# Kernel tuning notes

Measured on AMD Instinct MI355X. Metric: run time of the kernel, lower is better.

The kernel has to match this reference:

```python
import jax, jax.numpy as jnp
import numpy as np

NUM_TAGS = 5

def setup_inputs() -> dict:
    key = jax.random.key(0)
    ks = jax.random.split(key, 8)
    B, N, K, Q = 2, 5, 5, 4
    Ls, Lq, D = 128, 128, 768
    inp = {
        'support_token_embedding': jax.random.normal(ks[0], (B * N * K, Ls, D), jnp.float32),
        'query_token_embedding': jax.random.normal(ks[1], (B * N * Q, Lq, D), jnp.float32),
        'support_mask': jnp.ones((B * N * K, Ls), jnp.float32),
        'query_mask': jnp.ones((B * N * Q, Lq), jnp.float32),
        'support_entity_label': jax.random.normal(ks[2], (B * N * K, Ls, NUM_TAGS), jnp.float32),
        'proj_w': jax.random.normal(ks[3], (D, 4 * D), jnp.float32) * 0.02,
        'proj_b': jnp.zeros((D,), jnp.float32),
        'rel_w1': jax.random.normal(ks[4], (D, 4 * D), jnp.float32) * 0.02,
        'rel_b1': jnp.zeros((D,), jnp.float32),
        'rel_w2': jax.random.normal(ks[5], (1, D), jnp.float32) * 0.02,
        'rel_b2': jnp.zeros((1,), jnp.float32),
        'B': B, 'N': N, 'K': K, 'Q': Q,
    }
    return inp

def _fuse(m1, m2):
    return jnp.concatenate([m1, m2, jnp.abs(m1 - m2), m1 * m2], axis=-1)

def reference(support_token_embedding, query_token_embedding, support_mask, query_mask,
              support_entity_label, proj_w, proj_b, rel_w1, rel_b1, rel_w2, rel_b2,
              B, N, K, Q):
    D = support_token_embedding.shape[-1]
    Lq = query_token_embedding.shape[1]

    # ---- cal_bio: per-(sample,shot) tag prototypes, vectorized ----
    labels = jnp.argmax(support_entity_label, axis=-1)                 # [BNK, Ls]
    onehot = jax.nn.one_hot(labels, NUM_TAGS, dtype=jnp.float32)       # [BNK, Ls, T]
    # tag 0 ('O') is additionally gated by the support mask
    masks = jnp.concatenate([onehot[:, :, :1] * support_mask[:, :, None], onehot[:, :, 1:]], axis=2)
    sums = jnp.einsum('blt,bld->btd', masks, support_token_embedding)  # [BNK, T, D]
    cnt = jnp.sum(masks, axis=1)[:, :, None]                           # [BNK, T, 1]
    proto = jnp.where(cnt > 0, sums / jnp.maximum(cnt, 1.0), 0.0)      # [BNK, T, D]
    proto = proto.reshape(B * N, K, NUM_TAGS, D).mean(axis=1)          # mean over K shots
    proto = proto.reshape(B, N, NUM_TAGS, D)                           # support_BIO

    # ---- expand to all (query, class) pairs: batch = B*N*Q*N ----
    BQ = B * N * Q * N
    support = jnp.broadcast_to(proto[:, None], (B, N * Q, N, NUM_TAGS, D)).reshape(BQ, NUM_TAGS, D)
    query = jnp.broadcast_to(query_token_embedding.reshape(B, N * Q, 1, Lq, D),
                             (B, N * Q, N, Lq, D)).reshape(BQ, Lq, D)
    qmask = jnp.broadcast_to(query_mask.reshape(B, N * Q, 1, Lq),
                             (B, N * Q, N, Lq)).reshape(BQ, Lq, 1)
    smask = jnp.ones((BQ, NUM_TAGS, 1), jnp.float32)

    # ---- CoAttention with additive mask bias + post-softmax mask multiply ----
    att = jnp.einsum('bsd,bqd->bsq', support, query) + smask * jnp.swapaxes(qmask, 1, 2) * 100.0
    support_ = jnp.einsum('bsq,bqd->bsd', jax.nn.softmax(att, axis=2), query) * smask
    query_ = jnp.einsum('bqs,bsd->bqd', jax.nn.softmax(jnp.swapaxes(att, 1, 2), axis=2), support) * qmask

    # ---- fuse + proj + relu ----
    es = jax.nn.relu(_fuse(support, support_) @ proj_w.T + proj_b)     # [BQ, T, D]
    eq = jax.nn.relu(_fuse(query, query_) @ proj_w.T + proj_b)        # [BQ, Lq, D]

    # ---- local aggregation: masked max + mean pooling ----
    eq_agg = jnp.concatenate([jnp.max(eq, axis=1), jnp.sum(eq, axis=1) / jnp.sum(qmask, axis=1)], axis=1)
    es_agg = jnp.concatenate([jnp.max(es, axis=1), jnp.sum(es, axis=1) / jnp.sum(smask, axis=1)], axis=1)

    # ---- relation MLP ----
    cat_seq = jnp.concatenate([eq_agg, es_agg], axis=1)                # [BQ, 4D]
    h = jax.nn.relu(cat_seq @ rel_w1.T + rel_b1)
    logits = h @ rel_w2.T + rel_b2                                     # [BQ, 1]
    return logits.reshape(B * N * Q, N)
```

## Files before the change

### kernel.cpp

```cpp
#include <hip/hip_runtime.h>

typedef unsigned short u16;
typedef __attribute__((ext_vector_type(8))) short short8;
typedef __attribute__((ext_vector_type(4))) float f32x4;

#define B_   2
#define N_   5
#define K_   5
#define Q_   4
#define T_   5
#define D_   768
#define L_   128
#define BN_  (B_*N_)
#define BNK_ (B_*N_*K_)
#define BQ_  (B_*N_*Q_*N_)
#define K4_  (4*D_)
#define KF   2304
#define AROWS 144

#define QEMB_N  (40*128*768)
#define PROJW_N (768*3072)

__device__ __forceinline__ float bf2f(u16 u) {
    return __uint_as_float(((unsigned)u) << 16);
}
__device__ __forceinline__ u16 f2bf(float f) {
    unsigned u = __float_as_uint(f);
    return (u16)((u + 0x7fffu + ((u >> 16) & 1u)) >> 16);
}
__device__ __forceinline__ void gl_lds16(const u16* g, u16* l) {
    __builtin_amdgcn_global_load_lds(
        (const __attribute__((address_space(1))) unsigned int*)g,
        (__attribute__((address_space(3))) unsigned int*)l, 16, 0, 0);
}

__global__ void k_convert3(const float* __restrict__ q, const float* __restrict__ pw,
                           const float* __restrict__ rw, u16* __restrict__ qo,
                           u16* __restrict__ po, u16* __restrict__ ro) {
    const long n1 = QEMB_N / 4, n2 = PROJW_N / 4;
    const long total = n1 + 2 * n2;
    for (long i = (long)blockIdx.x * 256 + threadIdx.x; i < total; i += (long)gridDim.x * 256) {
        const float* src; u16* dst; long k;
        if (i < n1)            { src = q;  dst = qo; k = i; }
        else if (i < n1 + n2)  { src = pw; dst = po; k = i - n1; }
        else                   { src = rw; dst = ro; k = i - n1 - n2; }
        float4 v = ((const float4*)src)[k];
        u16 o[4] = {f2bf(v.x), f2bf(v.y), f2bf(v.z), f2bf(v.w)};
        *(uint2*)(dst + k * 4) = *(const uint2*)o;
    }
}

__global__ void k_proto_shot(const float* __restrict__ label, const float* __restrict__ smask,
                             const float* __restrict__ semb, float* __restrict__ proto_shot) {
    int bnk = blockIdx.x;
    __shared__ int   s_tag[L_];
    __shared__ float s_w[L_];
    __shared__ float s_cnt[T_];
    int tid = threadIdx.x;
    if (tid < L_) {
        const float* lp = label + ((long)bnk * L_ + tid) * T_;
        float best = lp[0]; int bi = 0;
        #pragma unroll
        for (int t = 1; t < T_; ++t) { float v = lp[t]; if (v > best) { best = v; bi = t; } }
        s_tag[tid] = bi;
        s_w[tid]   = (bi == 0) ? smask[(long)bnk * L_ + tid] : 1.0f;
    }
    __syncthreads();
    if (tid < T_) {
        float c = 0.f;
        for (int l = 0; l < L_; ++l) if (s_tag[l] == tid) c += s_w[l];
        s_cnt[tid] = c;
    }
    __syncthreads();
    float acc[3][T_] = {};
    for (int l = 0; l < L_; ++l) {
        float w = s_w[l]; int tg = s_tag[l];
        const float* ep = semb + ((long)bnk * L_ + l) * D_;
        #pragma unroll
        for (int s = 0; s < 3; ++s) {
            float e = ep[tid + s * 256] * w;
            #pragma unroll
            for (int t = 0; t < T_; ++t) acc[s][t] += (tg == t) ? e : 0.0f;
        }
    }
    #pragma unroll
    for (int s = 0; s < 3; ++s) {
        int d = tid + s * 256;
        #pragma unroll
        for (int t = 0; t < T_; ++t) {
            float c = s_cnt[t];
            float v = (c > 0.f) ? acc[s][t] / fmaxf(c, 1.f) : 0.f;
            proto_shot[(bnk * T_ + t) * D_ + d] = v;
        }
    }
}

__global__ void k_proto_mean(const float* __restrict__ proto_shot,
                             float* __restrict__ proto_f32, u16* __restrict__ proto_bf) {
    int idx = blockIdx.x * 256 + threadIdx.x;
    if (idx >= BN_ * T_ * D_) return;
    int bn = idx / (T_ * D_);
    int rem = idx - bn * (T_ * D_);
    float s = 0.f;
    #pragma unroll
    for (int k = 0; k < K_; ++k) s += proto_shot[(bn * K_ + k) * (T_ * D_) + rem];
    s *= (1.f / K_);
    proto_f32[idx] = s;
    proto_bf[idx]  = f2bf(s);
}

__global__ void k_attn(const float* __restrict__ qemb, const float* __restrict__ qmask_g,
                       const float* __restrict__ proto_f32,
                       u16* __restrict__ qf, float* __restrict__ qssum_ws) {
    int bq = blockIdx.x;
    int q_idx = bq / N_;
    int bn = (bq / (N_ * Q_ * N_)) * N_ + (bq % N_);
    __shared__ float s_proto[T_ * D_];
    __shared__ float s_att[T_][L_];
    __shared__ float s_ps[T_][L_];
    __shared__ float s_p2[L_][8];
    __shared__ float s_qm[L_];
    int tid = threadIdx.x;
    for (int i = tid; i < T_ * D_; i += 256) s_proto[i] = proto_f32[bn * T_ * D_ + i];
    if (tid < L_) s_qm[tid] = qmask_g[(long)q_idx * L_ + tid];
    __syncthreads();
    for (int p = tid; p < T_ * L_; p += 256) {
        int t = p >> 7, q = p & (L_ - 1);
        const float* pp = s_proto + t * D_;
        const float4* qp = (const float4*)(qemb + ((size_t)q_idx * L_ + q) * D_);
        float acc = 0.f;
        #pragma unroll 4
        for (int d = 0; d < D_ / 4; ++d) {
            float4 v = qp[d];
            acc += v.x * pp[4 * d] + v.y * pp[4 * d + 1] + v.z * pp[4 * d + 2] + v.w * pp[4 * d + 3];
        }
        s_att[t][q] = acc + 100.f * s_qm[q];
    }
    __syncthreads();
    if (tid < T_) {
        int t = tid; float m = -1e30f;
        for (int q = 0; q < L_; ++q) m = fmaxf(m, s_att[t][q]);
        float ss = 0.f;
        for (int q = 0; q < L_; ++q) { float e = __expf(s_att[t][q] - m); s_ps[t][q] = e; ss += e; }
        float inv = 1.f / ss;
        for (int q = 0; q < L_; ++q) s_ps[t][q] *= inv;
    } else if (tid >= 128) {
        int q = tid - 128; float m = -1e30f;
        float e[T_];
        #pragma unroll
        for (int t = 0; t < T_; ++t) m = fmaxf(m, s_att[t][q]);
        float ss = 0.f;
        #pragma unroll
        for (int t = 0; t < T_; ++t) { e[t] = __expf(s_att[t][q] - m); ss += e[t]; }
        float inv = s_qm[q] / ss;
        #pragma unroll
        for (int t = 0; t < T_; ++t) s_p2[q][t] = e[t] * inv;
    } else if (tid == 5) {
        float s = 0.f;
        for (int q = 0; q < L_; ++q) s += s_qm[q];
        qssum_ws[bq] = s;
    }
    __syncthreads();
    u16* qfb = qf + (size_t)bq * AROWS * KF;
    {
        float acc[T_][3] = {};
        #pragma unroll 4
        for (int q = 0; q < L_; ++q) {
            const float* qp = qemb + ((size_t)q_idx * L_ + q) * D_;
            float qv[3];
            #pragma unroll
            for (int s = 0; s < 3; ++s) qv[s] = qp[tid + s * 256];
            #pragma unroll
            for (int t = 0; t < T_; ++t) {
                float p = s_ps[t][q];
                #pragma unroll
                for (int s = 0; s < 3; ++s) acc[t][s] += p * qv[s];
            }
        }
        #pragma unroll
        for (int t = 0; t < T_; ++t) {
            u16* er = qfb + (128 + t) * KF;
            #pragma unroll
            for (int s = 0; s < 3; ++s) {
                int d = tid + s * 256;
                float p = s_proto[t * D_ + d];
                float sv = acc[t][s];
                er[d]            = f2bf(sv);
                er[768 + d]      = f2bf(fabsf(p - sv));
                er[1536 + d]     = f2bf(p * sv);
            }
        }
    }
    {
        int q = tid >> 1, h = tid & 1;
        float wt[T_];
        #pragma unroll
        for (int t = 0; t < T_; ++t) wt[t] = s_p2[q][t];
        const float* qrow = qemb + ((size_t)q_idx * L_ + q) * D_ + h * 384;
        u16* qr = qfb + q * KF + h * 384;
        for (int oct = 0; oct < 48; ++oct) {
            int d = h * 384 + oct * 8;
            float4 v0 = *(const float4*)(qrow + oct * 8);
            float4 v1 = *(const float4*)(qrow + oct * 8 + 4);
            float qv[8] = {v0.x, v0.y, v0.z, v0.w, v1.x, v1.y, v1.z, v1.w};
            float m2[8] = {0, 0, 0, 0, 0, 0, 0, 0};
            #pragma unroll
            for (int t = 0; t < T_; ++t) {
                float4 p0 = *(const float4*)(s_proto + t * D_ + d);
                float4 p1 = *(const float4*)(s_proto + t * D_ + d + 4);
                float w = wt[t];
                m2[0] += w * p0.x; m2[1] += w * p0.y; m2[2] += w * p0.z; m2[3] += w * p0.w;
                m2[4] += w * p1.x; m2[5] += w * p1.y; m2[6] += w * p1.z; m2[7] += w * p1.w;
            }
            short8 o1, o2, o3;
            #pragma unroll
            for (int i = 0; i < 8; ++i) {
                o1[i] = (short)f2bf(m2[i]);
                o2[i] = (short)f2bf(fabsf(qv[i] - m2[i]));
                o3[i] = (short)f2bf(qv[i] * m2[i]);
            }
            *(short8*)(qr + oct * 8)        = o1;
            *(short8*)(qr + 768 + oct * 8)  = o2;
            *(short8*)(qr + 1536 + oct * 8) = o3;
        }
    }
    {
        u16* pr = qfb + 133 * KF;
        short8 z = short8{0, 0, 0, 0, 0, 0, 0, 0};
        for (int i = tid; i < (11 * KF) / 8; i += 256) *(short8*)(pr + i * 8) = z;
    }
}

#define SWZ(g, r) (((g) << 4) + ((r) ^ ((g) << 2)))
__global__ __launch_bounds__(256) void k_gemm_g1(const u16* __restrict__ qemb_bf,
                                                 const u16* __restrict__ proto_bf,
                                                 const u16* __restrict__ projw_bf,
                                                 u16* __restrict__ g1) {
    int mbase = blockIdx.y * 128;
    int jbase = blockIdx.x * 128;
    __shared__ __align__(16) u16 sA[8 * 512];
    __shared__ __align__(16) u16 sB[8 * 512];
    int tid = threadIdx.x;
    int lane = tid & 63, w = tid >> 6, quad = lane >> 4, l16 = lane & 15;
    f32x4 zero = {0.f, 0.f, 0.f, 0.f};
    f32x4 acc[8][2];
    #pragma unroll
    for (int rt = 0; rt < 8; ++rt) { acc[rt][0] = zero; acc[rt][1] = zero; }

    for (int kt = 0; kt < 24; ++kt) {
        int k0 = kt * 32;
        __syncthreads();
        #pragma unroll
        for (int j = 0; j < 2; ++j) {
            int v = tid + j * 256, row = v >> 2, g = v & 3;
            *(uint4*)(sB + (((row >> 4) << 6) + SWZ(g, row & 15)) * 8) =
                *(const uint4*)(projw_bf + (size_t)(jbase + row) * K4_ + k0 + g * 8);
            int grow = mbase + row;
            uint4 av = uint4{0u, 0u, 0u, 0u};
            if (grow < 5120)      av = *(const uint4*)(qemb_bf + (size_t)grow * D_ + k0 + g * 8);
            else if (grow < 5170) av = *(const uint4*)(proto_bf + (size_t)(grow - 5120) * D_ + k0 + g * 8);
            *(uint4*)(sA + (((row >> 4) << 6) + SWZ(g, row & 15)) * 8) = av;
        }
        __syncthreads();
        short8 af[8], bfr[2];
        #pragma unroll
        for (int rt = 0; rt < 8; ++rt)
            af[rt] = *(const short8*)(sA + ((rt << 6) + SWZ(quad, l16)) * 8);
        #pragma unroll
        for (int jj = 0; jj < 2; ++jj)
            bfr[jj] = *(const short8*)(sB + (((w * 2 + jj) << 6) + SWZ(quad, l16)) * 8);
        #pragma unroll
        for (int rt = 0; rt < 8; ++rt)
            #pragma unroll
            for (int jj = 0; jj < 2; ++jj)
                acc[rt][jj] = __builtin_amdgcn_mfma_f32_16x16x32_bf16(af[rt], bfr[jj], acc[rt][jj], 0, 0, 0);
    }
    #pragma unroll
    for (int jj = 0; jj < 2; ++jj) {
        int col = jbase + (w * 2 + jj) * 16 + l16;
        #pragma unroll
        for (int rt = 0; rt < 8; ++rt)
            #pragma unroll
            for (int r = 0; r < 4; ++r) {
                int row = mbase + rt * 16 + quad * 4 + r;
                g1[(size_t)row * D_ + col] = f2bf(acc[rt][jj][r]);
            }
    }
}

__global__ __launch_bounds__(256) void k_gemm_q(
        const u16* __restrict__ qf, const u16* __restrict__ projw_bf,
        const float* __restrict__ projb, const u16* __restrict__ g1,
        const float* __restrict__ qssum_ws, u16* __restrict__ cat_ws) {
    int bq = blockIdx.x;
    int jbase = blockIdx.y * 128;
    int q_idx = bq / N_;
    int bn = (bq / (N_ * Q_ * N_)) * N_ + (bq % N_);
    __shared__ __align__(16) u16 sA[AROWS * 32];
    __shared__ __align__(16) u16 sB[128 * 32];
    int tid = threadIdx.x;
    int lane = tid & 63, w = tid >> 6, quad = lane >> 4, l16 = lane & 15;
    int srow = lane >> 2, sko = lane & 3;
    const u16* Ab = qf + (size_t)bq * AROWS * KF + (size_t)srow * KF + sko * 8;
    const u16* Bb = projw_bf + (size_t)jbase * K4_ + 768 + (size_t)srow * K4_ + sko * 8;
    u16* lA0 = sA + (w * 16) * 32;
    u16* lA1 = sA + (64 + w * 16) * 32;
    u16* lA2 = sA + 128 * 32;
    u16* lB0 = sB + (w * 16) * 32;
    u16* lB1 = sB + (64 + w * 16) * 32;

    f32x4 zero = {0.f, 0.f, 0.f, 0.f};
    f32x4 acc[9][2];
    #pragma unroll
    for (int rt = 0; rt < 9; ++rt) { acc[rt][0] = zero; acc[rt][1] = zero; }

    for (int kt = 0; kt < KF / 32; ++kt) {
        int k0 = kt * 32;
        __syncthreads();
        gl_lds16(Ab + (size_t)(w * 16) * KF + k0, lA0);
        gl_lds16(Ab + (size_t)(64 + w * 16) * KF + k0, lA1);
        if (w == 0) gl_lds16(Ab + (size_t)128 * KF + k0, lA2);
        gl_lds16(Bb + (size_t)(w * 16) * K4_ + k0, lB0);
        gl_lds16(Bb + (size_t)(64 + w * 16) * K4_ + k0, lB1);
        __syncthreads();
        short8 af[9], bfr[2];
        #pragma unroll
        for (int rt = 0; rt < 9; ++rt)
            af[rt] = *(const short8*)(sA + (rt * 16 + l16) * 32 + quad * 8);
        #pragma unroll
        for (int jj = 0; jj < 2; ++jj)
            bfr[jj] = *(const short8*)(sB + ((w * 2 + jj) * 16 + l16) * 32 + quad * 8);
        #pragma unroll
        for (int rt = 0; rt < 9; ++rt)
            #pragma unroll
            for (int jj = 0; jj < 2; ++jj)
                acc[rt][jj] = __builtin_amdgcn_mfma_f32_16x16x32_bf16(af[rt], bfr[jj], acc[rt][jj], 0, 0, 0);
    }
    float inv_qs = 1.f / qssum_ws[bq];
    #pragma unroll
    for (int jj = 0; jj < 2; ++jj) {
        int col = jbase + (w * 2 + jj) * 16 + l16;
        float bias = projb[col];
        float qmax = 0.f, qsum = 0.f, smax = 0.f, ssum = 0.f;
        #pragma unroll
        for (int rt = 0; rt < 8; ++rt) {
            #pragma unroll
            for (int r = 0; r < 4; ++r) {
                int row = rt * 16 + quad * 4 + r;
                float g1v = bf2f(g1[(size_t)(q_idx * 128 + row) * D_ + col]);
                float v = fmaxf(acc[rt][jj][r] + g1v + bias, 0.f);
                qmax = fmaxf(qmax, v); qsum += v;
            }
        }
        #pragma unroll
        for (int r = 0; r < 4; ++r) {
            int t = quad * 4 + r;
            if (t < T_) {
                float g1v = bf2f(g1[(size_t)(5120 + bn * T_ + t) * D_ + col]);
                float v = fmaxf(acc[8][jj][r] + g1v + bias, 0.f);
                smax = fmaxf(smax, v); ssum += v;
            }
        }
        qmax = fmaxf(qmax, __shfl_xor(qmax, 16, 64)); qmax = fmaxf(qmax, __shfl_xor(qmax, 32, 64));
        qsum += __shfl_xor(qsum, 16, 64);             qsum += __shfl_xor(qsum, 32, 64);
        smax = fmaxf(smax, __shfl_xor(smax, 16, 64)); smax = fmaxf(smax, __shfl_xor(smax, 32, 64));
        ssum += __shfl_xor(ssum, 16, 64);             ssum += __shfl_xor(ssum, 32, 64);
        if (quad == 0) {
            u16* cp = cat_ws + (size_t)bq * K4_;
            cp[col]           = f2bf(qmax);
            cp[D_ + col]      = f2bf(qsum * inv_qs);
            cp[2 * D_ + col]  = f2bf(smax);
            cp[3 * D_ + col]  = f2bf(ssum * 0.2f);
        }
    }
}

#define AST  40
__global__ __launch_bounds__(256) void k_relmlp(const u16* __restrict__ cat_ws,
                                                const u16* __restrict__ w1,
                                                float* __restrict__ part) {
    int mbase = blockIdx.y * 64;
    int jbase = blockIdx.x * 128;
    int ks = blockIdx.z;
    __shared__ __align__(16) u16 sA[64 * AST];
    __shared__ __align__(16) u16 sB[128 * AST];
    int tid = threadIdx.x;
    int lane = tid & 63, w = tid >> 6, quad = lane >> 4, l16 = lane & 15;
    f32x4 zero = {0.f, 0.f, 0.f, 0.f};
    f32x4 acc[4][2];
    #pragma unroll
    for (int rt = 0; rt < 4; ++rt) { acc[rt][0] = zero; acc[rt][1] = zero; }

    for (int kt = ks * 12; kt < ks * 12 + 12; ++kt) {
        int k0 = kt * 32;
        __syncthreads();
        {
            int row = tid >> 2, ko = (tid & 3) * 8;
            int grow = mbase + row;
            short8 val = short8{0, 0, 0, 0, 0, 0, 0, 0};
            if (grow < BQ_) val = *(const short8*)(cat_ws + (size_t)grow * K4_ + k0 + ko);
            *(short8*)(sA + row * AST + ko) = val;
        }
        for (int u = tid; u < 512; u += 256) {
            int row = u >> 2, ko = (u & 3) * 8;
            *(short8*)(sB + row * AST + ko) =
                *(const short8*)(w1 + (size_t)(jbase + row) * K4_ + k0 + ko);
        }
        __syncthreads();
        short8 af[4], bfr[2];
        #pragma unroll
        for (int rt = 0; rt < 4; ++rt)
            af[rt] = *(const short8*)(sA + (rt * 16 + l16) * AST + quad * 8);
        #pragma unroll
        for (int jj = 0; jj < 2; ++jj)
            bfr[jj] = *(const short8*)(sB + ((2 * w + jj) * 16 + l16) * AST + quad * 8);
        #pragma unroll
        for (int rt = 0; rt < 4; ++rt)
            #pragma unroll
            for (int jj = 0; jj < 2; ++jj)
                acc[rt][jj] = __builtin_amdgcn_mfma_f32_16x16x32_bf16(af[rt], bfr[jj], acc[rt][jj], 0, 0, 0);
    }
    #pragma unroll
    for (int jj = 0; jj < 2; ++jj) {
        int col = jbase + (2 * w + jj) * 16 + l16;
        #pragma unroll
        for (int rt = 0; rt < 4; ++rt) {
            #pragma unroll
            for (int r = 0; r < 4; ++r) {
                int grow = mbase + rt * 16 + quad * 4 + r;
                if (grow < BQ_)
                    part[((size_t)ks * BQ_ + grow) * D_ + col] = acc[rt][jj][r];
            }
        }
    }
}

__global__ void k_rel_fin(const float* __restrict__ part, const float* __restrict__ b1,
                          const float* __restrict__ w2, const float* __restrict__ b2,
                          float* __restrict__ out) {
    int bq = blockIdx.x, tid = threadIdx.x;
    float a = 0.f;
    #pragma unroll
    for (int s = 0; s < 3; ++s) {
        int col = tid + s * 256;
        float sum = 0.f;
        #pragma unroll
        for (int ks = 0; ks < 8; ++ks) sum += part[((size_t)ks * BQ_ + bq) * D_ + col];
        float h = fmaxf(sum + b1[col], 0.f);
        a += h * w2[col];
    }
    __shared__ float red[256];
    red[tid] = a; __syncthreads();
    for (int off = 128; off >= 1; off >>= 1) {
        if (tid < off) red[tid] += red[tid + off];
        __syncthreads();
    }
    if (tid == 0) out[bq] = red[0] + b2[0];
}

extern "C" void kernel_launch(void* const* d_in, const int* in_sizes, int n_in,
                              void* d_out, int out_size, void* d_ws, size_t ws_size,
                              hipStream_t stream) {
    (void)in_sizes; (void)n_in; (void)out_size; (void)ws_size;
    const float* semb  = (const float*)d_in[0];
    const float* qemb  = (const float*)d_in[1];
    const float* smask = (const float*)d_in[2];
    const float* qmask = (const float*)d_in[3];
    const float* label = (const float*)d_in[4];
    const float* projw = (const float*)d_in[5];
    const float* projb = (const float*)d_in[6];
    const float* relw1 = (const float*)d_in[7];
    const float* relb1 = (const float*)d_in[8];
    const float* relw2 = (const float*)d_in[9];
    const float* relb2 = (const float*)d_in[10];

    char* ws = (char*)d_ws;
    u16*   qemb_bf   = (u16*)  (ws + 0);
    u16*   projw_bf  = (u16*)  (ws + 7864320);
    u16*   relw1_bf  = (u16*)  (ws + 12582912);
    float* proto_shot= (float*)(ws + 17301504);
    float* proto_f32 = (float*)(ws + 18069504);
    u16*   proto_bf  = (u16*)  (ws + 18223104);
    float* qssum     = (float*)(ws + 18299904);
    u16*   cat_ws    = (u16*)  (ws + 18300800);
    u16*   g1_ws     = (u16*)  (ws + 19529600);
    float* part_ws   = (float*)(ws + 19529600);
    u16*   qf_ws     = (u16*)  (ws + 27590528);

    k_convert3<<<2048, 256, 0, stream>>>(qemb, projw, relw1, qemb_bf, projw_bf, relw1_bf);
    k_proto_shot<<<BNK_, 256, 0, stream>>>(label, smask, semb, proto_shot);
    k_proto_mean<<<150, 256, 0, stream>>>(proto_shot, proto_f32, proto_bf);
    k_attn<<<BQ_, 256, 0, stream>>>(qemb, qmask, proto_f32, qf_ws, qssum);
    k_gemm_g1<<<dim3(6, 41), 256, 0, stream>>>(qemb_bf, proto_bf, projw_bf, g1_ws);
    k_gemm_q<<<dim3(BQ_, 6), 256, 0, stream>>>(qf_ws, projw_bf, projb, g1_ws, qssum, cat_ws);
    k_relmlp<<<dim3(6, 4, 8), 256, 0, stream>>>(cat_ws, relw1_bf, part_ws);
    k_rel_fin<<<BQ_, 256, 0, stream>>>(part_ws, relb1, relw2, relb2, (float*)d_out);
}
```

Before: 567.5 us.

## Factor attended-support projection block out of per-pair GEMM via linearity

The query_ term (a softmax-weighted mix of the 5 prototypes) is no longer materialised per row and pushed through the projection GEMM. Because the projection is linear, the prototypes and attended supports are projected once in a new small GEMM, and the per-row contribution is rebuilt in the epilogue as a 5-term weighted sum. This shrinks the K dimension of the main per-pair GEMM from 2304 to 1536 and removes one third of the qf writes. It adds a kernel launch, extra workspace buffers, an epilogue mixing step and LDS staging, and the block indices are remapped so blocks sharing a query land on the same XCD.

```diff
diff --git a/kernel.cpp b/kernel.cpp
--- a/kernel.cpp
+++ b/kernel.cpp
@@ -15,7 +15,7 @@
 #define BNK_ (B_*N_*K_)
 #define BQ_  (B_*N_*Q_*N_)
 #define K4_  (4*D_)
-#define KF   2304
+#define KFQ  1536
 #define AROWS 144
 
 #define QEMB_N  (40*128*768)
@@ -111,9 +111,14 @@
 
 __global__ void k_attn(const float* __restrict__ qemb, const float* __restrict__ qmask_g,
                        const float* __restrict__ proto_f32,
-                       u16* __restrict__ qf, float* __restrict__ qssum_ws) {
-    int bq = blockIdx.x;
-    int q_idx = bq / N_;
+                       u16* __restrict__ qf, u16* __restrict__ sup_ws,
+                       float* __restrict__ p2m_ws, float* __restrict__ qssum_ws) {
+    int x = blockIdx.x;
+    int xcd = x & 7, slot = x >> 3;
+    int g = (slot / 5) * 8 + xcd;
+    int n2 = slot % 5;
+    int bq = g * 5 + n2;
+    int q_idx = g;
     int bn = (bq / (N_ * Q_ * N_)) * N_ + (bq % N_);
     __shared__ float s_proto[T_ * D_];
     __shared__ float s_att[T_][L_];
@@ -121,6 +126,7 @@
     __shared__ float s_p2[L_][8];
     __shared__ float s_qm[L_];
     int tid = threadIdx.x;
+    int w = tid >> 6, lane = tid & 63;
     for (int i = tid; i < T_ * D_; i += 256) s_proto[i] = proto_f32[bn * T_ * D_ + i];
     if (tid < L_) s_qm[tid] = qmask_g[(long)q_idx * L_ + tid];
     __syncthreads();
@@ -154,14 +160,17 @@
         for (int t = 0; t < T_; ++t) { e[t] = __expf(s_att[t][q] - m); ss += e[t]; }
         float inv = s_qm[q] / ss;
         #pragma unroll
-        for (int t = 0; t < T_; ++t) s_p2[q][t] = e[t] * inv;
+        for (int t = 0; t < T_; ++t) {
+            s_p2[q][t] = e[t] * inv;
+            p2m_ws[((size_t)bq * T_ + t) * L_ + q] = e[t] * inv;
+        }
     } else if (tid == 5) {
         float s = 0.f;
         for (int q = 0; q < L_; ++q) s += s_qm[q];
         qssum_ws[bq] = s;
     }
     __syncthreads();
-    u16* qfb = qf + (size_t)bq * AROWS * KF;
+    u16* qfb = qf + (size_t)bq * AROWS * KFQ;
     {
         float acc[T_][3] = {};
         #pragma unroll 4
@@ -179,55 +188,50 @@
         }
         #pragma unroll
         for (int t = 0; t < T_; ++t) {
-            u16* er = qfb + (128 + t) * KF;
+            u16* er = qfb + (size_t)(128 + t) * KFQ;
             #pragma unroll
             for (int s = 0; s < 3; ++s) {
                 int d = tid + s * 256;
                 float p = s_proto[t * D_ + d];
                 float sv = acc[t][s];
-                er[d]            = f2bf(sv);
-                er[768 + d]      = f2bf(fabsf(p - sv));
-                er[1536 + d]     = f2bf(p * sv);
+                sup_ws[((size_t)bq * T_ + t) * D_ + d] = f2bf(sv);
+                er[d]       = f2bf(fabsf(p - sv));
+                er[768 + d] = f2bf(p * sv);
+            }
+        }
+    }
+    for (int rr = 0; rr < 32; ++rr) {
+        int row = w * 32 + rr;
+        float p0 = s_p2[row][0], p1 = s_p2[row][1], p2v = s_p2[row][2];
+        float p3 = s_p2[row][3], p4 = s_p2[row][4];
+        const float* qrow = qemb + ((size_t)q_idx * L_ + row) * D_;
+        u16* qr = qfb + (size_t)row * KFQ;
+        #pragma unroll
+        for (int pass = 0; pass < 2; ++pass) {
+            int u = lane + pass * 64;
+            if (u < 96) {
+                int d = u * 8;
+                float4 a0 = *(const float4*)(qrow + d);
+                float4 a1 = *(const float4*)(qrow + d + 4);
+                float qv[8] = {a0.x, a0.y, a0.z, a0.w, a1.x, a1.y, a1.z, a1.w};
+                short8 o2, o3;
+                #pragma unroll
+                for (int i = 0; i < 8; ++i) {
+                    float m2 = p0 * s_proto[d + i] + p1 * s_proto[D_ + d + i]
+                             + p2v * s_proto[2 * D_ + d + i] + p3 * s_proto[3 * D_ + d + i]
+                             + p4 * s_proto[4 * D_ + d + i];
+                    o2[i] = (short)f2bf(fabsf(qv[i] - m2));
+                    o3[i] = (short)f2bf(qv[i] * m2);
+                }
+                *(short8*)(qr + d)       = o2;
+                *(short8*)(qr + 768 + d) = o3;
             }
         }
     }
     {
-        int q = tid >> 1, h = tid & 1;
-        float wt[T_];
-        #pragma unroll
-        for (int t = 0; t < T_; ++t) wt[t] = s_p2[q][t];
-        const float* qrow = qemb + ((size_t)q_idx * L_ + q) * D_ + h * 384;
-        u16* qr = qfb + q * KF + h * 384;
-        for (int oct = 0; oct < 48; ++oct) {
-            int d = h * 384 + oct * 8;
-            float4 v0 = *(const float4*)(qrow + oct * 8);
-            float4 v1 = *(const float4*)(qrow + oct * 8 + 4);
-            float qv[8] = {v0.x, v0.y, v0.z, v0.w, v1.x, v1.y, v1.z, v1.w};
-            float m2[8] = {0, 0, 0, 0, 0, 0, 0, 0};
-            #pragma unroll
-            for (int t = 0; t < T_; ++t) {
-                float4 p0 = *(const float4*)(s_proto + t * D_ + d);
-                float4 p1 = *(const float4*)(s_proto + t * D_ + d + 4);
-                float w = wt[t];
-                m2[0] += w * p0.x; m2[1] += w * p0.y; m2[2] += w * p0.z; m2[3] += w * p0.w;
-                m2[4] += w * p1.x; m2[5] += w * p1.y; m2[6] += w * p1.z; m2[7] += w * p1.w;
-            }
-            short8 o1, o2, o3;
-            #pragma unroll
-            for (int i = 0; i < 8; ++i) {
-                o1[i] = (short)f2bf(m2[i]);
-                o2[i] = (short)f2bf(fabsf(qv[i] - m2[i]));
-                o3[i] = (short)f2bf(qv[i] * m2[i]);
-            }
-            *(short8*)(qr + oct * 8)        = o1;
-            *(short8*)(qr + 768 + oct * 8)  = o2;
-            *(short8*)(qr + 1536 + oct * 8) = o3;
-        }
-    }
-    {
-        u16* pr = qfb + 133 * KF;
+        u16* pr = qfb + (size_t)133 * KFQ;
         short8 z = short8{0, 0, 0, 0, 0, 0, 0, 0};
-        for (int i = tid; i < (11 * KF) / 8; i += 256) *(short8*)(pr + i * 8) = z;
+        for (int i = tid; i < (11 * KFQ) / 8; i += 256) *(short8*)(pr + i * 8) = z;
     }
 }
 
@@ -288,21 +292,84 @@
     }
 }
 
+__global__ __launch_bounds__(256) void k_gemm_w2(const u16* __restrict__ sup_ws,
+                                                 const u16* __restrict__ proto_bf,
+                                                 const u16* __restrict__ projw_bf,
+                                                 u16* __restrict__ sw2, u16* __restrict__ pw2) {
+    int mbase = blockIdx.y * 128;
+    int jbase = blockIdx.x * 128;
+    __shared__ __align__(16) u16 sA[8 * 512];
+    __shared__ __align__(16) u16 sB[8 * 512];
+    int tid = threadIdx.x;
+    int lane = tid & 63, w = tid >> 6, quad = lane >> 4, l16 = lane & 15;
+    f32x4 zero = {0.f, 0.f, 0.f, 0.f};
+    f32x4 acc[8][2];
+    #pragma unroll
+    for (int rt = 0; rt < 8; ++rt) { acc[rt][0] = zero; acc[rt][1] = zero; }
+
+    for (int kt = 0; kt < 24; ++kt) {
+        int k0 = kt * 32;
+        __syncthreads();
+        #pragma unroll
+        for (int j = 0; j < 2; ++j) {
+            int v = tid + j * 256, row = v >> 2, g = v & 3;
+            *(uint4*)(sB + (((row >> 4) << 6) + SWZ(g, row & 15)) * 8) =
+                *(const uint4*)(projw_bf + (size_t)(jbase + row) * K4_ + 768 + k0 + g * 8);
+            int grow = mbase + row;
+            uint4 av = uint4{0u, 0u, 0u, 0u};
+            if (grow < 1000)      av = *(const uint4*)(sup_ws + (size_t)grow * D_ + k0 + g * 8);
+            else if (grow < 1050) av = *(const uint4*)(proto_bf + (size_t)(grow - 1000) * D_ + k0 + g * 8);
+            *(uint4*)(sA + (((row >> 4) << 6) + SWZ(g, row & 15)) * 8) = av;
+        }
+        __syncthreads();
+        short8 af[8], bfr[2];
+        #pragma unroll
+        for (int rt = 0; rt < 8; ++rt)
+            af[rt] = *(const short8*)(sA + ((rt << 6) + SWZ(quad, l16)) * 8);
+        #pragma unroll
+        for (int jj = 0; jj < 2; ++jj)
+            bfr[jj] = *(const short8*)(sB + (((w * 2 + jj) << 6) + SWZ(quad, l16)) * 8);
+        #pragma unroll
+        for (int rt = 0; rt < 8; ++rt)
+            #pragma unroll
+            for (int jj = 0; jj < 2; ++jj)
+                acc[rt][jj] = __builtin_amdgcn_mfma_f32_16x16x32_bf16(af[rt], bfr[jj], acc[rt][jj], 0, 0, 0);
+    }
+    #pragma unroll
+    for (int jj = 0; jj < 2; ++jj) {
+        int col = jbase + (w * 2 + jj) * 16 + l16;
+        #pragma unroll
+        for (int rt = 0; rt < 8; ++rt)
+            #pragma unroll
+            for (int r = 0; r < 4; ++r) {
+                int row = mbase + rt * 16 + quad * 4 + r;
+                if (row < 1000)      sw2[(size_t)row * D_ + col] = f2bf(acc[rt][jj][r]);
+                else if (row < 1050) pw2[(size_t)(row - 1000) * D_ + col] = f2bf(acc[rt][jj][r]);
+            }
+    }
+}
+
 __global__ __launch_bounds__(256) void k_gemm_q(
         const u16* __restrict__ qf, const u16* __restrict__ projw_bf,
         const float* __restrict__ projb, const u16* __restrict__ g1,
-        const float* __restrict__ qssum_ws, u16* __restrict__ cat_ws) {
-    int bq = blockIdx.x;
-    int jbase = blockIdx.y * 128;
+        const u16* __restrict__ pw2, const u16* __restrict__ sw2,
+        const float* __restrict__ p2m, const float* __restrict__ qssum_ws,
+        u16* __restrict__ cat_ws) {
+    int x = blockIdx.x;
+    int xcd = x & 7, slot = x >> 3;
+    int bq = (slot / 6) * 8 + xcd;
+    int jbase = (slot % 6) * 128;
     int q_idx = bq / N_;
     int bn = (bq / (N_ * Q_ * N_)) * N_ + (bq % N_);
     __shared__ __align__(16) u16 sA[AROWS * 32];
     __shared__ __align__(16) u16 sB[128 * 32];
+    __shared__ float s_p2mL[T_ * 128];
+    __shared__ float s_pw2L[T_ * 128];
     int tid = threadIdx.x;
     int lane = tid & 63, w = tid >> 6, quad = lane >> 4, l16 = lane & 15;
     int srow = lane >> 2, sko = lane & 3;
-    const u16* Ab = qf + (size_t)bq * AROWS * KF + (size_t)srow * KF + sko * 8;
-    const u16* Bb = projw_bf + (size_t)jbase * K4_ + 768 + (size_t)srow * K4_ + sko * 8;
+    const u16* Ab = qf + (size_t)bq * AROWS * KFQ + (size_t)srow * KFQ + sko * 8;
+    const u16* Bb = projw_bf + (size_t)jbase * K4_ + 1536 + (size_t)srow * K4_ + sko * 8;
     u16* lA0 = sA + (w * 16) * 32;
     u16* lA1 = sA + (64 + w * 16) * 32;
     u16* lA2 = sA + 128 * 32;
@@ -314,12 +381,12 @@
     #pragma unroll
     for (int rt = 0; rt < 9; ++rt) { acc[rt][0] = zero; acc[rt][1] = zero; }
 
-    for (int kt = 0; kt < KF / 32; ++kt) {
+    for (int kt = 0; kt < KFQ / 32; ++kt) {
         int k0 = kt * 32;
         __syncthreads();
-        gl_lds16(Ab + (size_t)(w * 16) * KF + k0, lA0);
-        gl_lds16(Ab + (size_t)(64 + w * 16) * KF + k0, lA1);
-        if (w == 0) gl_lds16(Ab + (size_t)128 * KF + k0, lA2);
+        gl_lds16(Ab + (size_t)(w * 16) * KFQ + k0, lA0);
+        gl_lds16(Ab + (size_t)(64 + w * 16) * KFQ + k0, lA1);
+        if (w == 0) gl_lds16(Ab + (size_t)128 * KFQ + k0, lA2);
         gl_lds16(Bb + (size_t)(w * 16) * K4_ + k0, lB0);
         gl_lds16(Bb + (size_t)(64 + w * 16) * K4_ + k0, lB1);
         __syncthreads();
@@ -336,10 +403,16 @@
             for (int jj = 0; jj < 2; ++jj)
                 acc[rt][jj] = __builtin_amdgcn_mfma_f32_16x16x32_bf16(af[rt], bfr[jj], acc[rt][jj], 0, 0, 0);
     }
+    for (int i = tid; i < T_ * 128; i += 256) {
+        s_p2mL[i] = p2m[(size_t)bq * (T_ * 128) + i];
+        s_pw2L[i] = bf2f(pw2[(size_t)(bn * T_ + (i >> 7)) * D_ + jbase + (i & 127)]);
+    }
+    __syncthreads();
     float inv_qs = 1.f / qssum_ws[bq];
     #pragma unroll
     for (int jj = 0; jj < 2; ++jj) {
         int col = jbase + (w * 2 + jj) * 16 + l16;
+        int cj = (w * 2 + jj) * 16 + l16;
         float bias = projb[col];
         float qmax = 0.f, qsum = 0.f, smax = 0.f, ssum = 0.f;
         #pragma unroll
@@ -348,7 +421,12 @@
             for (int r = 0; r < 4; ++r) {
                 int row = rt * 16 + quad * 4 + r;
                 float g1v = bf2f(g1[(size_t)(q_idx * 128 + row) * D_ + col]);
-                float v = fmaxf(acc[rt][jj][r] + g1v + bias, 0.f);
+                float mix = s_p2mL[row] * s_pw2L[cj]
+                          + s_p2mL[128 + row] * s_pw2L[128 + cj]
+                          + s_p2mL[256 + row] * s_pw2L[256 + cj]
+                          + s_p2mL[384 + row] * s_pw2L[384 + cj]
+                          + s_p2mL[512 + row] * s_pw2L[512 + cj];
+                float v = fmaxf(acc[rt][jj][r] + g1v + mix + bias, 0.f);
                 qmax = fmaxf(qmax, v); qsum += v;
             }
         }
@@ -357,7 +435,8 @@
             int t = quad * 4 + r;
             if (t < T_) {
                 float g1v = bf2f(g1[(size_t)(5120 + bn * T_ + t) * D_ + col]);
-                float v = fmaxf(acc[8][jj][r] + g1v + bias, 0.f);
+                float s2v = bf2f(sw2[(size_t)(bq * T_ + t) * D_ + col]);
+                float v = fmaxf(acc[8][jj][r] + g1v + s2v + bias, 0.f);
                 smax = fmaxf(smax, v); ssum += v;
             }
         }
@@ -482,17 +561,23 @@
     float* proto_f32 = (float*)(ws + 18069504);
     u16*   proto_bf  = (u16*)  (ws + 18223104);
     float* qssum     = (float*)(ws + 18299904);
-    u16*   cat_ws    = (u16*)  (ws + 18300800);
-    u16*   g1_ws     = (u16*)  (ws + 19529600);
-    float* part_ws   = (float*)(ws + 19529600);
-    u16*   qf_ws     = (u16*)  (ws + 27590528);
+    u16*   sup_ws    = (u16*)  (ws + 18300800);
+    float* p2m_ws    = (float*)(ws + 19836800);
+    u16*   pw2_ws    = (u16*)  (ws + 20348800);
+    u16*   sw2_ws    = (u16*)  (ws + 20425600);
+    u16*   cat_ws    = (u16*)  (ws + 21961600);
+    u16*   g1_ws     = (u16*)  (ws + 23190400);
+    float* part_ws   = (float*)(ws + 31251328);
+    u16*   qf_ws     = (u16*)  (ws + 36166528);
 
     k_convert3<<<2048, 256, 0, stream>>>(qemb, projw, relw1, qemb_bf, projw_bf, relw1_bf);
     k_proto_shot<<<BNK_, 256, 0, stream>>>(label, smask, semb, proto_shot);
     k_proto_mean<<<150, 256, 0, stream>>>(proto_shot, proto_f32, proto_bf);
-    k_attn<<<BQ_, 256, 0, stream>>>(qemb, qmask, proto_f32, qf_ws, qssum);
+    k_attn<<<BQ_, 256, 0, stream>>>(qemb, qmask, proto_f32, qf_ws, sup_ws, p2m_ws, qssum);
     k_gemm_g1<<<dim3(6, 41), 256, 0, stream>>>(qemb_bf, proto_bf, projw_bf, g1_ws);
-    k_gemm_q<<<dim3(BQ_, 6), 256, 0, stream>>>(qf_ws, projw_bf, projb, g1_ws, qssum, cat_ws);
+    k_gemm_w2<<<dim3(6, 9), 256, 0, stream>>>(sup_ws, proto_bf, projw_bf, sw2_ws, pw2_ws);
+    k_gemm_q<<<1200, 256, 0, stream>>>(qf_ws, projw_bf, projb, g1_ws, pw2_ws, sw2_ws,
+                                       p2m_ws, qssum, cat_ws);
     k_relmlp<<<dim3(6, 4, 8), 256, 0, stream>>>(cat_ws, relw1_bf, part_ws);
     k_rel_fin<<<BQ_, 256, 0, stream>>>(part_ws, relb1, relw2, relb2, (float*)d_out);
 }
```

New measurement: 536.6 us. 1.06x faster.
